# Kernel optimization log

Measured on AMD Instinct MI355X. Metric: run time of the kernel, lower is better.

The kernel has to match this reference:

```python
import jax, jax.numpy as jnp
import numpy as np

N_T = 100000   # transaction nodes
N_A = 50000    # account nodes
F = 256        # raw feature dim
H = 256        # hidden_dim
E = 800000     # edges per edge type


def setup_inputs() -> dict:
    key = jax.random.key(0)
    ks = jax.random.split(key, 14)
    s = 1.0 / np.sqrt(F)
    return {
        "x_tx": jax.random.normal(ks[0], (N_T, F), jnp.float32),
        "x_acc": jax.random.normal(ks[1], (N_A, F), jnp.float32),
        "edge_at_src": jax.random.randint(ks[2], (E,), 0, N_A, jnp.int32),
        "edge_at_dst": jax.random.randint(ks[3], (E,), 0, N_T, jnp.int32),
        "edge_ta_src": jax.random.randint(ks[4], (E,), 0, N_T, jnp.int32),
        "edge_ta_dst": jax.random.randint(ks[5], (E,), 0, N_A, jnp.int32),
        "W_l_at": jax.random.normal(ks[6], (F, H), jnp.float32) * s,
        "b_l_at": jnp.zeros((H,), jnp.float32),
        "W_r_at": jax.random.normal(ks[7], (F, H), jnp.float32) * s,
        "W_l_ta": jax.random.normal(ks[8], (F, H), jnp.float32) * s,
        "b_l_ta": jnp.zeros((H,), jnp.float32),
        "W_r_ta": jax.random.normal(ks[9], (F, H), jnp.float32) * s,
        "W_out": jax.random.normal(ks[10], (H, 1), jnp.float32) * (1.0 / np.sqrt(H)),
        "b_out": jnp.zeros((1,), jnp.float32),
    }


def _sage(x_src, x_dst, src_idx, dst_idx, W_l, b_l, W_r, num_dst):
    # PyG SAGEConv (mean aggr): lin_l(mean_j x_src[j]) + lin_r(x_dst)
    msgs = x_src[src_idx]  # [E, F] gather
    summed = jax.ops.segment_sum(msgs, dst_idx, num_segments=num_dst)  # [num_dst, F]
    cnt = jax.ops.segment_sum(jnp.ones((src_idx.shape[0],), x_src.dtype), dst_idx,
                              num_segments=num_dst)
    mean = summed / jnp.maximum(cnt, 1.0)[:, None]  # isolated dst -> zeros
    return mean @ W_l + b_l + x_dst @ W_r


def reference(x_tx, x_acc, edge_at_src, edge_at_dst, edge_ta_src, edge_ta_dst,
              W_l_at, b_l_at, W_r_at, W_l_ta, b_l_ta, W_r_ta, W_out, b_out):
    # account -> transaction SAGEConv
    h_tx = _sage(x_acc, x_tx, edge_at_src, edge_at_dst, W_l_at, b_l_at, W_r_at, N_T)
    # transaction -> account SAGEConv (computed as in HeteroConv, though unused downstream)
    h_acc = _sage(x_tx, x_acc, edge_ta_src, edge_ta_dst, W_l_ta, b_l_ta, W_r_ta, N_A)
    tx_x = jax.nn.relu(h_tx)
    _ = jax.nn.relu(h_acc)
    logits = (tx_x @ W_out + b_out)[:, 0]  # squeeze(-1)
    return logits, tx_x
```

## Files before the change

kernel.cpp:

```cpp
#include <hip/hip_runtime.h>
#include <hip/hip_bf16.h>

typedef __bf16 bf16x8_t __attribute__((ext_vector_type(8)));
typedef __bf16 bf16x4_t __attribute__((ext_vector_type(4)));
typedef float f32x4_t __attribute__((ext_vector_type(4)));

#define M_TX 100000
#define N_AC 50000
#define FDIM 256
#define HDIM 256
#define KTOT 512
#define SCAN_NBLK ((M_TX + 1023) / 1024)

__device__ inline bf16x8_t bzero8() {
    bf16x8_t v;
#pragma unroll
    for (int z = 0; z < 8; ++z) v[z] = (__bf16)0.f;
    return v;
}

__global__ __launch_bounds__(256) void initk2(float* __restrict__ logits,
                                              int* __restrict__ hist,
                                              int* __restrict__ fill,
                                              const float* __restrict__ b_out) {
    int i = blockIdx.x * 256 + threadIdx.x;
    if (i < M_TX) {
        logits[i] = b_out[0];
        hist[i] = 0;
        fill[i] = 0;
    }
}

__global__ __launch_bounds__(256) void transw(const float* __restrict__ Wl,
                                              const float* __restrict__ Wr,
                                              __bf16* __restrict__ WT) {
    int t = blockIdx.x * 256 + threadIdx.x;
    if (t >= FDIM * HDIM) return;
    int k = t >> 8;
    int n = t & 255;
    WT[n * KTOT + k]        = (__bf16)Wl[k * HDIM + n];
    WT[n * KTOT + 256 + k]  = (__bf16)Wr[k * HDIM + n];
}

__global__ __launch_bounds__(256) void cvtk(const float* __restrict__ src,
                                            __bf16* __restrict__ dst, int n4) {
    int stride = gridDim.x * 256;
    for (int i = blockIdx.x * 256 + threadIdx.x; i < n4; i += stride) {
        f32x4_t v = ((const f32x4_t*)src)[i];
        bf16x4_t w;
        w[0] = (__bf16)v.x; w[1] = (__bf16)v.y;
        w[2] = (__bf16)v.z; w[3] = (__bf16)v.w;
        ((bf16x4_t*)dst)[i] = w;
    }
}

__global__ __launch_bounds__(256) void histk(const int* __restrict__ edst,
                                             int* __restrict__ hist, int E) {
    int e = blockIdx.x * 256 + threadIdx.x;
    if (e >= E) return;
    atomicAdd(&hist[edst[e]], 1);
}

__global__ __launch_bounds__(1024) void scan1k(const int* __restrict__ hist,
                                               int* __restrict__ row_start,
                                               int* __restrict__ partials) {
    __shared__ int tmp[1024];
    const int b = blockIdx.x;
    const int t = threadIdx.x;
    const int i = b * 1024 + t;
    int v = (i < M_TX) ? hist[i] : 0;
    tmp[t] = v;
    __syncthreads();
    for (int off = 1; off < 1024; off <<= 1) {
        int u = (t >= off) ? tmp[t - off] : 0;
        __syncthreads();
        tmp[t] += u;
        __syncthreads();
    }
    if (i < M_TX) row_start[i] = tmp[t] - v;
    if (t == 1023) partials[b] = tmp[1023];
}

__global__ __launch_bounds__(128) void scan2k(int* __restrict__ partials,
                                              int* __restrict__ row_start) {
    __shared__ int tmp[128];
    const int t = threadIdx.x;
    int v = (t < SCAN_NBLK) ? partials[t] : 0;
    tmp[t] = v;
    __syncthreads();
    for (int off = 1; off < 128; off <<= 1) {
        int u = (t >= off) ? tmp[t - off] : 0;
        __syncthreads();
        tmp[t] += u;
        __syncthreads();
    }
    if (t < SCAN_NBLK) partials[t] = tmp[t] - v;
    if (t == 127) row_start[M_TX] = tmp[127];
}

__global__ __launch_bounds__(1024) void scan3k(int* __restrict__ row_start,
                                               const int* __restrict__ partials) {
    const int i = blockIdx.x * 1024 + threadIdx.x;
    if (i < M_TX) row_start[i] += partials[blockIdx.x];
}

__global__ __launch_bounds__(256) void scatterk(const int* __restrict__ esrc,
                                                const int* __restrict__ edst,
                                                const int* __restrict__ row_start,
                                                int* __restrict__ fill,
                                                int* __restrict__ sorted_src, int E) {
    int e = blockIdx.x * 256 + threadIdx.x;
    if (e >= E) return;
    int d = edst[e];
    int pos = row_start[d] + atomicAdd(&fill[d], 1);
    sorted_src[pos] = esrc[e];
}

__global__ __launch_bounds__(256) void gatherk(const float* __restrict__ x_acc,
                                               const __bf16* __restrict__ xab,
                                               const int* __restrict__ sorted_src,
                                               const int* __restrict__ row_start,
                                               float* __restrict__ summed,
                                               __bf16* __restrict__ meanb) {
    int gw = (blockIdx.x * 256 + threadIdx.x) >> 6;
    if (gw >= M_TX) return;
    int lane = threadIdx.x & 63;
    int start = row_start[gw];
    int end = row_start[gw + 1];
    f32x4_t acc = {0.f, 0.f, 0.f, 0.f};
    if (xab) {
        for (int base = start; base < end; base += 64) {
            int n = end - base; if (n > 64) n = 64;
            int s = 0;
            if (base + lane < end) s = sorted_src[base + lane];
            for (int j = 0; j < n; ++j) {
                int sj = __shfl(s, j);
                const bf16x4_t v = *(const bf16x4_t*)(xab + (long)sj * FDIM + lane * 4);
                acc.x += (float)v[0]; acc.y += (float)v[1];
                acc.z += (float)v[2]; acc.w += (float)v[3];
            }
        }
    } else {
        for (int base = start; base < end; base += 64) {
            int n = end - base; if (n > 64) n = 64;
            int s = 0;
            if (base + lane < end) s = sorted_src[base + lane];
            for (int j = 0; j < n; ++j) {
                int sj = __shfl(s, j);
                const f32x4_t v = *(const f32x4_t*)(x_acc + (long)sj * FDIM + lane * 4);
                acc.x += v.x; acc.y += v.y; acc.z += v.z; acc.w += v.w;
            }
        }
    }
    if (meanb) {
        float inv = 1.0f / fmaxf((float)(end - start), 1.0f);
        bf16x4_t w;
        w[0] = (__bf16)(acc.x * inv); w[1] = (__bf16)(acc.y * inv);
        w[2] = (__bf16)(acc.z * inv); w[3] = (__bf16)(acc.w * inv);
        *(bf16x4_t*)(meanb + (long)gw * FDIM + lane * 4) = w;
    } else {
        *(f32x4_t*)(summed + (long)gw * FDIM + lane * 4) = acc;
    }
}

__global__ __launch_bounds__(512) void gemmk(const float* __restrict__ x_tx,
                                             const __bf16* __restrict__ xtb,
                                             const float* __restrict__ summed,
                                             const __bf16* __restrict__ meanb,
                                             const int* __restrict__ row_start,
                                             const __bf16* __restrict__ WT,
                                             const float* __restrict__ b_l,
                                             const float* __restrict__ W_out,
                                             float* __restrict__ tx_out,
                                             float* __restrict__ logits) {
    __shared__ __bf16 As[128][72];
    __shared__ __bf16 Bs[256][72];

    const int m0 = blockIdx.x * 128;
    const int tid = threadIdx.x;
    const int wid = tid >> 6;
    const int lane = tid & 63;
    const int wm = wid >> 2;
    const int wn = wid & 3;
    const int lc = lane & 15;
    const int lr = lane >> 4;

    f32x4_t acc[4][4];
#pragma unroll
    for (int i = 0; i < 4; ++i)
#pragma unroll
        for (int j = 0; j < 4; ++j) acc[i][j] = (f32x4_t){0.f, 0.f, 0.f, 0.f};

    const int ar = tid >> 2;
    const int acq = tid & 3;
    const int arm = m0 + ar;
    const bool arow_ok = arm < M_TX;
    float invc = 1.0f;
    if (!meanb) {
        int idx = arow_ok ? arm : (M_TX - 1);
        int c = row_start[idx + 1] - row_start[idx];
        invc = 1.0f / fmaxf((float)c, 1.0f);
    }

    for (int kc = 0; kc < 8; ++kc) {
        __syncthreads();
        {
            const bool first = kc < 4;
            const int kb = (kc & 3) * 64;
            const __bf16* bsrc = first ? meanb : xtb;
            if (bsrc) {
                const __bf16* bb = bsrc + (long)arm * FDIM + kb + acq * 16;
                bf16x8_t v0 = bzero8(), v1 = bzero8();
                if (arow_ok) {
                    v0 = *(const bf16x8_t*)bb;
                    v1 = *(const bf16x8_t*)(bb + 8);
                }
                *(bf16x8_t*)(&As[ar][acq * 16]) = v0;
                *(bf16x8_t*)(&As[ar][acq * 16 + 8]) = v1;
            } else {
                const float sc = first ? invc : 1.0f;
                const float* base = first ? (summed + (long)arm * FDIM + kb)
                                          : (x_tx + (long)arm * FDIM + kb);
#pragma unroll
                for (int c4 = 0; c4 < 4; ++c4) {
                    int kk = acq * 16 + c4 * 4;
                    f32x4_t v = {0.f, 0.f, 0.f, 0.f};
                    if (arow_ok) v = *(const f32x4_t*)(base + kk);
                    bf16x4_t w;
                    w[0] = (__bf16)(v.x * sc);
                    w[1] = (__bf16)(v.y * sc);
                    w[2] = (__bf16)(v.z * sc);
                    w[3] = (__bf16)(v.w * sc);
                    *(bf16x4_t*)(&As[ar][kk]) = w;
                }
            }
        }
#pragma unroll
        for (int i = 0; i < 4; ++i) {
            int t2 = tid + i * 512;
            int n = t2 >> 3;
            int c = t2 & 7;
            bf16x8_t v = *(const bf16x8_t*)(WT + n * KTOT + kc * 64 + c * 8);
            *(bf16x8_t*)(&Bs[n][c * 8]) = v;
        }
        __syncthreads();
        const int kfr = lr * 8;
#pragma unroll
        for (int kk = 0; kk < 2; ++kk) {
            bf16x8_t af[4], bfr[4];
#pragma unroll
            for (int f = 0; f < 4; ++f) {
                af[f] = *(const bf16x8_t*)(&As[wm * 64 + f * 16 + lc][kk * 32 + kfr]);
                bfr[f] = *(const bf16x8_t*)(&Bs[wn * 64 + f * 16 + lc][kk * 32 + kfr]);
            }
#pragma unroll
            for (int fm = 0; fm < 4; ++fm)
#pragma unroll
                for (int fn = 0; fn < 4; ++fn)
                    acc[fm][fn] = __builtin_amdgcn_mfma_f32_16x16x32_bf16(
                        af[fm], bfr[fn], acc[fm][fn], 0, 0, 0);
        }
    }

    float wout[4], bl[4];
#pragma unroll
    for (int fn = 0; fn < 4; ++fn) {
        int col = wn * 64 + fn * 16 + lc;
        wout[fn] = W_out[col];
        bl[fn] = b_l[col];
    }
#pragma unroll
    for (int fm = 0; fm < 4; ++fm) {
        float part[4] = {0.f, 0.f, 0.f, 0.f};
#pragma unroll
        for (int fn = 0; fn < 4; ++fn) {
            int col = wn * 64 + fn * 16 + lc;
#pragma unroll
            for (int r = 0; r < 4; ++r) {
                int row = m0 + wm * 64 + fm * 16 + lr * 4 + r;
                float h = acc[fm][fn][r] + bl[fn];
                h = fmaxf(h, 0.0f);
                if (row < M_TX) tx_out[(long)row * HDIM + col] = h;
                part[r] += h * wout[fn];
            }
        }
#pragma unroll
        for (int r = 0; r < 4; ++r) {
            float p = part[r];
            p += __shfl_xor(p, 1);
            p += __shfl_xor(p, 2);
            p += __shfl_xor(p, 4);
            p += __shfl_xor(p, 8);
            int row = m0 + wm * 64 + fm * 16 + lr * 4 + r;
            if (lc == 0 && row < M_TX) unsafeAtomicAdd(logits + row, p);
        }
    }
}

extern "C" void kernel_launch(void* const* d_in, const int* in_sizes, int n_in,
                              void* d_out, int out_size, void* d_ws, size_t ws_size,
                              hipStream_t stream) {
    const float* x_tx  = (const float*)d_in[0];
    const float* x_acc = (const float*)d_in[1];
    const int* e_src   = (const int*)d_in[2];
    const int* e_dst   = (const int*)d_in[3];
    const float* W_l   = (const float*)d_in[6];
    const float* b_l   = (const float*)d_in[7];
    const float* W_r   = (const float*)d_in[8];
    const float* W_out = (const float*)d_in[12];
    const float* b_out = (const float*)d_in[13];

    float* out = (float*)d_out;
    float* logits = out;
    float* summed = out + M_TX;

    char* ws = (char*)d_ws;
    size_t off = 0;
    auto alloc = [&](size_t bytes) {
        size_t o = off;
        off = (off + bytes + 255) & ~(size_t)255;
        return o;
    };
    size_t o_WT       = alloc((size_t)HDIM * KTOT * 2);
    size_t o_rowstart = alloc(((size_t)M_TX + 1) * 4);
    size_t o_fill     = alloc((size_t)M_TX * 4);
    size_t o_sorted   = alloc((size_t)800000 * 4);
    size_t o_hist     = alloc((size_t)M_TX * 4);
    size_t o_part     = alloc((size_t)SCAN_NBLK * 4);
    size_t base_end   = off;
    size_t o_xa       = alloc((size_t)N_AC * FDIM * 2);
    size_t lvlA_end   = off;
    size_t o_mean     = alloc((size_t)M_TX * FDIM * 2);
    size_t lvlB_end   = off;
    size_t o_xt       = alloc((size_t)M_TX * FDIM * 2);
    size_t lvlC_end   = off;
    (void)base_end;

    __bf16* WT       = (__bf16*)(ws + o_WT);
    int* row_start   = (int*)(ws + o_rowstart);
    int* fill        = (int*)(ws + o_fill);
    int* sorted_src  = (int*)(ws + o_sorted);
    int* histp       = (int*)(ws + o_hist);
    int* partials    = (int*)(ws + o_part);

    const bool lvlA = ws_size >= lvlA_end;
    const bool lvlB = ws_size >= lvlB_end;
    const bool lvlC = ws_size >= lvlC_end;
    __bf16* xab   = lvlA ? (__bf16*)(ws + o_xa)   : nullptr;
    __bf16* meanb = lvlB ? (__bf16*)(ws + o_mean) : nullptr;
    __bf16* xtb   = lvlC ? (__bf16*)(ws + o_xt)   : nullptr;

    const int E = in_sizes[2];

    hipLaunchKernelGGL(initk2, dim3((M_TX + 255) / 256), dim3(256), 0, stream,
                       logits, histp, fill, b_out);
    hipLaunchKernelGGL(transw, dim3((FDIM * HDIM + 255) / 256), dim3(256), 0, stream,
                       W_l, W_r, WT);
    if (xab)
        hipLaunchKernelGGL(cvtk, dim3(2048), dim3(256), 0, stream,
                           x_acc, xab, N_AC * FDIM / 4);
    if (xtb)
        hipLaunchKernelGGL(cvtk, dim3(2048), dim3(256), 0, stream,
                           x_tx, xtb, M_TX * FDIM / 4);
    hipLaunchKernelGGL(histk, dim3((E + 255) / 256), dim3(256), 0, stream,
                       e_dst, histp, E);
    hipLaunchKernelGGL(scan1k, dim3(SCAN_NBLK), dim3(1024), 0, stream,
                       histp, row_start, partials);
    hipLaunchKernelGGL(scan2k, dim3(1), dim3(128), 0, stream, partials, row_start);
    hipLaunchKernelGGL(scan3k, dim3(SCAN_NBLK), dim3(1024), 0, stream,
                       row_start, partials);
    hipLaunchKernelGGL(scatterk, dim3((E + 255) / 256), dim3(256), 0, stream,
                       e_src, e_dst, row_start, fill, sorted_src, E);
    hipLaunchKernelGGL(gatherk, dim3(M_TX / 4), dim3(256), 0, stream,
                       x_acc, xab, sorted_src, row_start, summed, meanb);
    hipLaunchKernelGGL(gemmk, dim3((M_TX + 127) / 128), dim3(512), 0, stream,
                       x_tx, xtb, summed, meanb, row_start, WT, b_l, W_out,
                       out + M_TX, logits);
}
```

Measured before the change: 462.8 us.

## Fuse setup kernels, widen gather loads, and register-prefetch GEMM tiles

Merges the weight transpose into the init kernel and the two bf16 conversion kernels into one launch, cutting launch count. The gather kernel gets a bf16 path where each half-wave handles alternate edges with 16-byte loads, reducing the two halves with a cross-lane xor shuffle. The GEMM prefetches the next K-chunk of A and B into registers while the current chunk runs through MFMA, so global load latency overlaps compute. The cost is higher register pressure in the GEMM and extra shuffle/branch work in the gather.

```diff
diff --git a/kernel.cpp b/kernel.cpp
--- a/kernel.cpp
+++ b/kernel.cpp
@@ -19,27 +19,44 @@
     return v;
 }
 
-__global__ __launch_bounds__(256) void initk2(float* __restrict__ logits,
+__global__ __launch_bounds__(256) void initk3(float* __restrict__ logits,
                                               int* __restrict__ hist,
                                               int* __restrict__ fill,
-                                              const float* __restrict__ b_out) {
+                                              const float* __restrict__ b_out,
+                                              const float* __restrict__ Wl,
+                                              const float* __restrict__ Wr,
+                                              __bf16* __restrict__ WT) {
     int i = blockIdx.x * 256 + threadIdx.x;
     if (i < M_TX) {
         logits[i] = b_out[0];
         hist[i] = 0;
         fill[i] = 0;
     }
-}
-
-__global__ __launch_bounds__(256) void transw(const float* __restrict__ Wl,
-                                              const float* __restrict__ Wr,
-                                              __bf16* __restrict__ WT) {
-    int t = blockIdx.x * 256 + threadIdx.x;
-    if (t >= FDIM * HDIM) return;
-    int k = t >> 8;
-    int n = t & 255;
-    WT[n * KTOT + k]        = (__bf16)Wl[k * HDIM + n];
-    WT[n * KTOT + 256 + k]  = (__bf16)Wr[k * HDIM + n];
+    if (i < FDIM * HDIM) {
+        int k = i >> 8;
+        int n = i & 255;
+        WT[n * KTOT + k]       = (__bf16)Wl[k * HDIM + n];
+        WT[n * KTOT + 256 + k] = (__bf16)Wr[k * HDIM + n];
+    }
+}
+
+__global__ __launch_bounds__(256) void cvt2k(const float* __restrict__ s1,
+                                             __bf16* __restrict__ d1, int n4_1,
+                                             const float* __restrict__ s2,
+                                             __bf16* __restrict__ d2, int n4_2) {
+    int stride = gridDim.x * 256;
+    int tot = n4_1 + n4_2;
+    for (int i = blockIdx.x * 256 + threadIdx.x; i < tot; i += stride) {
+        const f32x4_t* sp;
+        bf16x4_t* dp;
+        if (i < n4_1) { sp = (const f32x4_t*)s1 + i; dp = (bf16x4_t*)d1 + i; }
+        else          { sp = (const f32x4_t*)s2 + (i - n4_1); dp = (bf16x4_t*)d2 + (i - n4_1); }
+        f32x4_t v = *sp;
+        bf16x4_t w;
+        w[0] = (__bf16)v.x; w[1] = (__bf16)v.y;
+        w[2] = (__bf16)v.z; w[3] = (__bf16)v.w;
+        *dp = w;
+    }
 }
 
 __global__ __launch_bounds__(256) void cvtk(const float* __restrict__ src,
@@ -127,6 +144,42 @@
     int lane = threadIdx.x & 63;
     int start = row_start[gw];
     int end = row_start[gw + 1];
+    if (xab && meanb) {
+        const int l5 = lane & 31;
+        const int half = lane >> 5;
+        f32x4_t a0 = {0.f, 0.f, 0.f, 0.f}, a1 = {0.f, 0.f, 0.f, 0.f};
+        for (int base = start; base < end; base += 64) {
+            int n = end - base; if (n > 64) n = 64;
+            int s = 0;
+            if (base + lane < end) s = sorted_src[base + lane];
+            int np = (n + 1) >> 1;
+            for (int j2 = 0; j2 < np; ++j2) {
+                int idx = 2 * j2 + half;
+                int sj = __shfl(s, idx);
+                if (idx < n) {
+                    bf16x8_t v = *(const bf16x8_t*)(xab + (long)sj * FDIM + l5 * 8);
+                    a0.x += (float)v[0]; a0.y += (float)v[1];
+                    a0.z += (float)v[2]; a0.w += (float)v[3];
+                    a1.x += (float)v[4]; a1.y += (float)v[5];
+                    a1.z += (float)v[6]; a1.w += (float)v[7];
+                }
+            }
+        }
+        a0.x += __shfl_xor(a0.x, 32); a0.y += __shfl_xor(a0.y, 32);
+        a0.z += __shfl_xor(a0.z, 32); a0.w += __shfl_xor(a0.w, 32);
+        a1.x += __shfl_xor(a1.x, 32); a1.y += __shfl_xor(a1.y, 32);
+        a1.z += __shfl_xor(a1.z, 32); a1.w += __shfl_xor(a1.w, 32);
+        if (half == 0) {
+            float inv = 1.0f / fmaxf((float)(end - start), 1.0f);
+            bf16x8_t w;
+            w[0] = (__bf16)(a0.x * inv); w[1] = (__bf16)(a0.y * inv);
+            w[2] = (__bf16)(a0.z * inv); w[3] = (__bf16)(a0.w * inv);
+            w[4] = (__bf16)(a1.x * inv); w[5] = (__bf16)(a1.y * inv);
+            w[6] = (__bf16)(a1.z * inv); w[7] = (__bf16)(a1.w * inv);
+            *(bf16x8_t*)(meanb + (long)gw * FDIM + l5 * 8) = w;
+        }
+        return;
+    }
     f32x4_t acc = {0.f, 0.f, 0.f, 0.f};
     if (xab) {
         for (int base = start; base < end; base += 64) {
@@ -195,29 +248,70 @@
     const int acq = tid & 3;
     const int arm = m0 + ar;
     const bool arow_ok = arm < M_TX;
-    float invc = 1.0f;
-    if (!meanb) {
-        int idx = arow_ok ? arm : (M_TX - 1);
-        int c = row_start[idx + 1] - row_start[idx];
-        invc = 1.0f / fmaxf((float)c, 1.0f);
-    }
-
-    for (int kc = 0; kc < 8; ++kc) {
-        __syncthreads();
+
+    if (meanb && xtb) {
+        bf16x8_t pa0, pa1, pb[4];
         {
-            const bool first = kc < 4;
-            const int kb = (kc & 3) * 64;
-            const __bf16* bsrc = first ? meanb : xtb;
-            if (bsrc) {
-                const __bf16* bb = bsrc + (long)arm * FDIM + kb + acq * 16;
-                bf16x8_t v0 = bzero8(), v1 = bzero8();
-                if (arow_ok) {
-                    v0 = *(const bf16x8_t*)bb;
-                    v1 = *(const bf16x8_t*)(bb + 8);
+            const __bf16* bb = meanb + (long)arm * FDIM + acq * 16;
+            pa0 = bzero8(); pa1 = bzero8();
+            if (arow_ok) { pa0 = *(const bf16x8_t*)bb; pa1 = *(const bf16x8_t*)(bb + 8); }
+#pragma unroll
+            for (int i = 0; i < 4; ++i) {
+                int t2 = tid + i * 512;
+                pb[i] = *(const bf16x8_t*)(WT + (t2 >> 3) * KTOT + (t2 & 7) * 8);
+            }
+        }
+        for (int kc = 0; kc < 8; ++kc) {
+            __syncthreads();
+            *(bf16x8_t*)(&As[ar][acq * 16]) = pa0;
+            *(bf16x8_t*)(&As[ar][acq * 16 + 8]) = pa1;
+#pragma unroll
+            for (int i = 0; i < 4; ++i) {
+                int t2 = tid + i * 512;
+                *(bf16x8_t*)(&Bs[t2 >> 3][(t2 & 7) * 8]) = pb[i];
+            }
+            __syncthreads();
+            if (kc < 7) {
+                int kn = kc + 1;
+                const __bf16* bsrc = (kn < 4) ? meanb : xtb;
+                const __bf16* bb = bsrc + (long)arm * FDIM + ((kn & 3) * 64) + acq * 16;
+                pa0 = bzero8(); pa1 = bzero8();
+                if (arow_ok) { pa0 = *(const bf16x8_t*)bb; pa1 = *(const bf16x8_t*)(bb + 8); }
+#pragma unroll
+                for (int i = 0; i < 4; ++i) {
+                    int t2 = tid + i * 512;
+                    pb[i] = *(const bf16x8_t*)(WT + (t2 >> 3) * KTOT + kn * 64 + (t2 & 7) * 8);
                 }
-                *(bf16x8_t*)(&As[ar][acq * 16]) = v0;
-                *(bf16x8_t*)(&As[ar][acq * 16 + 8]) = v1;
-            } else {
+            }
+            const int kfr = lr * 8;
+#pragma unroll
+            for (int kk = 0; kk < 2; ++kk) {
+                bf16x8_t af[4], bfr[4];
+#pragma unroll
+                for (int f = 0; f < 4; ++f) {
+                    af[f] = *(const bf16x8_t*)(&As[wm * 64 + f * 16 + lc][kk * 32 + kfr]);
+                    bfr[f] = *(const bf16x8_t*)(&Bs[wn * 64 + f * 16 + lc][kk * 32 + kfr]);
+                }
+#pragma unroll
+                for (int fm = 0; fm < 4; ++fm)
+#pragma unroll
+                    for (int fn = 0; fn < 4; ++fn)
+                        acc[fm][fn] = __builtin_amdgcn_mfma_f32_16x16x32_bf16(
+                            af[fm], bfr[fn], acc[fm][fn], 0, 0, 0);
+            }
+        }
+    } else {
+        float invc = 1.0f;
+        {
+            int idx = arow_ok ? arm : (M_TX - 1);
+            int c = row_start[idx + 1] - row_start[idx];
+            invc = 1.0f / fmaxf((float)c, 1.0f);
+        }
+        for (int kc = 0; kc < 8; ++kc) {
+            __syncthreads();
+            {
+                const bool first = kc < 4;
+                const int kb = (kc & 3) * 64;
                 const float sc = first ? invc : 1.0f;
                 const float* base = first ? (summed + (long)arm * FDIM + kb)
                                           : (x_tx + (long)arm * FDIM + kb);
@@ -234,31 +328,31 @@
                     *(bf16x4_t*)(&As[ar][kk]) = w;
                 }
             }
-        }
-#pragma unroll
-        for (int i = 0; i < 4; ++i) {
-            int t2 = tid + i * 512;
-            int n = t2 >> 3;
-            int c = t2 & 7;
-            bf16x8_t v = *(const bf16x8_t*)(WT + n * KTOT + kc * 64 + c * 8);
-            *(bf16x8_t*)(&Bs[n][c * 8]) = v;
-        }
-        __syncthreads();
-        const int kfr = lr * 8;
-#pragma unroll
-        for (int kk = 0; kk < 2; ++kk) {
-            bf16x8_t af[4], bfr[4];
-#pragma unroll
-            for (int f = 0; f < 4; ++f) {
-                af[f] = *(const bf16x8_t*)(&As[wm * 64 + f * 16 + lc][kk * 32 + kfr]);
-                bfr[f] = *(const bf16x8_t*)(&Bs[wn * 64 + f * 16 + lc][kk * 32 + kfr]);
-            }
-#pragma unroll
-            for (int fm = 0; fm < 4; ++fm)
-#pragma unroll
-                for (int fn = 0; fn < 4; ++fn)
-                    acc[fm][fn] = __builtin_amdgcn_mfma_f32_16x16x32_bf16(
-                        af[fm], bfr[fn], acc[fm][fn], 0, 0, 0);
+#pragma unroll
+            for (int i = 0; i < 4; ++i) {
+                int t2 = tid + i * 512;
+                int n = t2 >> 3;
+                int c = t2 & 7;
+                bf16x8_t v = *(const bf16x8_t*)(WT + n * KTOT + kc * 64 + c * 8);
+                *(bf16x8_t*)(&Bs[n][c * 8]) = v;
+            }
+            __syncthreads();
+            const int kfr = lr * 8;
+#pragma unroll
+            for (int kk = 0; kk < 2; ++kk) {
+                bf16x8_t af[4], bfr[4];
+#pragma unroll
+                for (int f = 0; f < 4; ++f) {
+                    af[f] = *(const bf16x8_t*)(&As[wm * 64 + f * 16 + lc][kk * 32 + kfr]);
+                    bfr[f] = *(const bf16x8_t*)(&Bs[wn * 64 + f * 16 + lc][kk * 32 + kfr]);
+                }
+#pragma unroll
+                for (int fm = 0; fm < 4; ++fm)
+#pragma unroll
+                    for (int fn = 0; fn < 4; ++fn)
+                        acc[fm][fn] = __builtin_amdgcn_mfma_f32_16x16x32_bf16(
+                            af[fm], bfr[fn], acc[fm][fn], 0, 0, 0);
+            }
         }
     }
 
@@ -327,14 +421,12 @@
     size_t o_sorted   = alloc((size_t)800000 * 4);
     size_t o_hist     = alloc((size_t)M_TX * 4);
     size_t o_part     = alloc((size_t)SCAN_NBLK * 4);
-    size_t base_end   = off;
     size_t o_xa       = alloc((size_t)N_AC * FDIM * 2);
     size_t lvlA_end   = off;
     size_t o_mean     = alloc((size_t)M_TX * FDIM * 2);
     size_t lvlB_end   = off;
     size_t o_xt       = alloc((size_t)M_TX * FDIM * 2);
     size_t lvlC_end   = off;
-    (void)base_end;
 
     __bf16* WT       = (__bf16*)(ws + o_WT);
     int* row_start   = (int*)(ws + o_rowstart);
@@ -352,16 +444,14 @@
 
     const int E = in_sizes[2];
 
-    hipLaunchKernelGGL(initk2, dim3((M_TX + 255) / 256), dim3(256), 0, stream,
-                       logits, histp, fill, b_out);
-    hipLaunchKernelGGL(transw, dim3((FDIM * HDIM + 255) / 256), dim3(256), 0, stream,
-                       W_l, W_r, WT);
-    if (xab)
+    hipLaunchKernelGGL(initk3, dim3((M_TX + 255) / 256), dim3(256), 0, stream,
+                       logits, histp, fill, b_out, W_l, W_r, WT);
+    if (xab && xtb)
+        hipLaunchKernelGGL(cvt2k, dim3(2048), dim3(256), 0, stream,
+                           x_acc, xab, N_AC * FDIM / 4, x_tx, xtb, M_TX * FDIM / 4);
+    else if (xab)
         hipLaunchKernelGGL(cvtk, dim3(2048), dim3(256), 0, stream,
                            x_acc, xab, N_AC * FDIM / 4);
-    if (xtb)
-        hipLaunchKernelGGL(cvtk, dim3(2048), dim3(256), 0, stream,
-                           x_tx, xtb, M_TX * FDIM / 4);
     hipLaunchKernelGGL(histk, dim3((E + 255) / 256), dim3(256), 0, stream,
                        e_dst, histp, E);
     hipLaunchKernelGGL(scan1k, dim3(SCAN_NBLK), dim3(1024), 0, stream,
```

Result: faster. 450.5 us (-2.7%).
